# Optimization experiments

Hardware: AMD Instinct MI355X
Metric: run time of the kernel (lower is better)

## Reference

```python
import jax, jax.numpy as jnp
import numpy as np

B, DK, N, DV = 16, 64, 8192, 64


def setup_inputs() -> dict:
    key = jax.random.key(0)
    kq, kk, kv = jax.random.split(key, 3)
    q = jax.random.normal(kq, (B, DK, N), dtype=jnp.float32)   # channel-first q
    k = jax.random.normal(kk, (B, N, DK), dtype=jnp.float32)
    v = jax.random.normal(kv, (B, N, DV), dtype=jnp.float32)
    return {"q": q, "k": k, "v": v}


def reference(q, k, v):
    # torch: bmm(q.permute(0,2,1), bmm(k.permute(0,2,1), v))
    # k^T v: [B, DK, DV] -- small on-chip-able intermediate
    ktv = jnp.einsum('bnk,bnv->bkv', k, v)
    # q^T (k^T v): [B, N, DV]
    out = jnp.einsum('bkn,bkv->bnv', q, ktv)
    return out
```

## Files before the change

kernel.cpp:

```cpp
#include <hip/hip_runtime.h>


#define B_   16
#define N_   8192
#define DK_  64
#define DV_  64

__global__ __launch_bounds__(256) void p1_partial(
    const float* __restrict__ K, const float* __restrict__ V,
    float* __restrict__ part, int rows_per_chunk)
{
    const int c = blockIdx.x;
    const int b = blockIdx.y;
    const int t = threadIdx.x;
    const int n0 = c * rows_per_chunk;

    const float* Kb = K + ((size_t)b * N_ + n0) * DK_;
    const float* Vb = V + ((size_t)b * N_ + n0) * DV_;

    __shared__ float sK[64 * 64];
    __shared__ float sV[64 * 64];

    const int kk4 = (t >> 4) * 4;
    const int vv4 = (t & 15) * 4;

    float acc[4][4] = {};

    for (int s = 0; s < rows_per_chunk; s += 64) {
        const float4* Ks = (const float4*)(Kb + (size_t)s * DK_);
        const float4* Vs = (const float4*)(Vb + (size_t)s * DV_);
        float4* sK4 = (float4*)sK;
        float4* sV4 = (float4*)sV;
        __syncthreads();
        #pragma unroll
        for (int i = t; i < 1024; i += 256) {
            sK4[i] = Ks[i];
            sV4[i] = Vs[i];
        }
        __syncthreads();

        #pragma unroll 8
        for (int n = 0; n < 64; ++n) {
            const float4 fk = *(const float4*)&sK[n * 64 + kk4];
            const float4 fv = *(const float4*)&sV[n * 64 + vv4];
            acc[0][0] += fk.x * fv.x; acc[0][1] += fk.x * fv.y;
            acc[0][2] += fk.x * fv.z; acc[0][3] += fk.x * fv.w;
            acc[1][0] += fk.y * fv.x; acc[1][1] += fk.y * fv.y;
            acc[1][2] += fk.y * fv.z; acc[1][3] += fk.y * fv.w;
            acc[2][0] += fk.z * fv.x; acc[2][1] += fk.z * fv.y;
            acc[2][2] += fk.z * fv.z; acc[2][3] += fk.z * fv.w;
            acc[3][0] += fk.w * fv.x; acc[3][1] += fk.w * fv.y;
            acc[3][2] += fk.w * fv.z; acc[3][3] += fk.w * fv.w;
        }
    }

    float* P = part + ((size_t)c * B_ + b) * 4096;
    #pragma unroll
    for (int i = 0; i < 4; ++i) {
        *(float4*)&P[(kk4 + i) * 64 + vv4] =
            make_float4(acc[i][0], acc[i][1], acc[i][2], acc[i][3]);
    }
}

__global__ __launch_bounds__(256) void p1_reduce(
    const float* __restrict__ part, float* __restrict__ ktv, int chunks)
{
    const int i = blockIdx.x * 256 + threadIdx.x;
    float4 s = make_float4(0.f, 0.f, 0.f, 0.f);
    for (int c = 0; c < chunks; ++c) {
        const float4 p = ((const float4*)part)[(size_t)c * 16384 + i];
        s.x += p.x; s.y += p.y; s.z += p.z; s.w += p.w;
    }
    ((float4*)ktv)[i] = s;
}

__global__ __launch_bounds__(256) void p2(
    const float* __restrict__ q, const float* __restrict__ ktv,
    float* __restrict__ out)
{
    const int nb = blockIdx.x;
    const int b  = blockIdx.y;
    const int t  = threadIdx.x;
    const int n0 = nb * 128;

    __shared__ float qs[64 * 128];
    __shared__ float ks[64 * 64];

    const float4* kt4 = (const float4*)(ktv + (size_t)b * 4096);
    #pragma unroll
    for (int i = t; i < 1024; i += 256) ((float4*)ks)[i] = kt4[i];

    const float* qb = q + (size_t)b * DK_ * N_ + n0;
    #pragma unroll
    for (int i = t; i < 2048; i += 256) {
        const int k  = i >> 5;
        const int c4 = i & 31;
        ((float4*)&qs[k * 128])[c4] = *(const float4*)&qb[(size_t)k * N_ + c4 * 4];
    }
    __syncthreads();

    const int nl = (t >> 4) * 8;
    const int vl = (t & 15) * 4;

    float acc[8][4] = {};

    #pragma unroll 4
    for (int k = 0; k < 64; ++k) {
        const float4 kv = *(const float4*)&ks[k * 64 + vl];
        float qn[8];
        *(float4*)&qn[0] = *(const float4*)&qs[k * 128 + nl];
        *(float4*)&qn[4] = *(const float4*)&qs[k * 128 + nl + 4];
        #pragma unroll
        for (int i = 0; i < 8; ++i) {
            acc[i][0] += qn[i] * kv.x;
            acc[i][1] += qn[i] * kv.y;
            acc[i][2] += qn[i] * kv.z;
            acc[i][3] += qn[i] * kv.w;
        }
    }

    float* ob = out + ((size_t)b * N_ + n0 + nl) * DV_ + vl;
    #pragma unroll
    for (int i = 0; i < 8; ++i) {
        *(float4*)&ob[(size_t)i * DV_] =
            make_float4(acc[i][0], acc[i][1], acc[i][2], acc[i][3]);
    }
}

extern "C" void kernel_launch(void* const* d_in, const int* in_sizes, int n_in,
                              void* d_out, int out_size, void* d_ws, size_t ws_size,
                              hipStream_t stream)
{
    const float* q = (const float*)d_in[0];
    const float* k = (const float*)d_in[1];
    const float* v = (const float*)d_in[2];
    float* out = (float*)d_out;

    int chunks = 32;
    while (chunks > 1 &&
           (size_t)(chunks + 1) * B_ * 4096 * sizeof(float) > ws_size)
        chunks >>= 1;
    const int rows_per_chunk = N_ / chunks;

    float* part = (float*)d_ws;
    float* ktv  = part + (size_t)chunks * B_ * 4096;

    p1_partial<<<dim3(chunks, B_), 256, 0, stream>>>(k, v, part, rows_per_chunk);
    p1_reduce<<<dim3(64), 256, 0, stream>>>(part, ktv, chunks);
    p2<<<dim3(64, B_), 256, 0, stream>>>(q, ktv, out);
}
```

Baseline: 161.3 us.

## Use 8x8 register tiles, double-buffered K/V loads and in-block wave reduction

```diff
diff --git a/kernel.cpp b/kernel.cpp
--- a/kernel.cpp
+++ b/kernel.cpp
@@ -1,73 +1,108 @@
 #include <hip/hip_runtime.h>
 
 
-#define B_   16
-#define N_   8192
-#define DK_  64
-#define DV_  64
+#define B_      16
+#define N_      8192
+#define DK_     64
+#define DV_     64
+#define CHUNKS_ 32
+#define ROWS_   256
+#define SUB_    4
 
 __global__ __launch_bounds__(256) void p1_partial(
     const float* __restrict__ K, const float* __restrict__ V,
-    float* __restrict__ part, int rows_per_chunk)
+    float* __restrict__ part)
 {
-    const int c = blockIdx.x;
-    const int b = blockIdx.y;
-    const int t = threadIdx.x;
-    const int n0 = c * rows_per_chunk;
+    __shared__ float sm[4][4096];
 
-    const float* Kb = K + ((size_t)b * N_ + n0) * DK_;
-    const float* Vb = V + ((size_t)b * N_ + n0) * DV_;
+    const int c = blockIdx.x, b = blockIdx.y, t = threadIdx.x;
+    const int w = t >> 6, lane = t & 63;
+    const int kk = (lane >> 3) * 8;
+    const int vv = (lane & 7) * 8;
 
-    __shared__ float sK[64 * 64];
-    __shared__ float sV[64 * 64];
+    const float4* K4 = (const float4*)(K + ((size_t)b * N_ + (size_t)c * ROWS_) * DK_);
+    const float4* V4 = (const float4*)(V + ((size_t)b * N_ + (size_t)c * ROWS_) * DV_);
 
-    const int kk4 = (t >> 4) * 4;
-    const int vv4 = (t & 15) * 4;
+    #pragma unroll
+    for (int j = 0; j < 4; ++j) {
+        ((float4*)sm[0])[t + 256 * j] = K4[t + 256 * j];
+        ((float4*)sm[1])[t + 256 * j] = V4[t + 256 * j];
+    }
+    __syncthreads();
 
-    float acc[4][4] = {};
+    float acc[8][8] = {};
 
-    for (int s = 0; s < rows_per_chunk; s += 64) {
-        const float4* Ks = (const float4*)(Kb + (size_t)s * DK_);
-        const float4* Vs = (const float4*)(Vb + (size_t)s * DV_);
-        float4* sK4 = (float4*)sK;
-        float4* sV4 = (float4*)sV;
-        __syncthreads();
+    for (int s = 0; s < SUB_; ++s) {
+        float4 nk[4], nv[4];
+        if (s + 1 < SUB_) {
+            const float4* Kn = K4 + (size_t)(s + 1) * 1024;
+            const float4* Vn = V4 + (size_t)(s + 1) * 1024;
+            #pragma unroll
+            for (int j = 0; j < 4; ++j) {
+                nk[j] = Kn[t + 256 * j];
+                nv[j] = Vn[t + 256 * j];
+            }
+        }
+
+        const float* cK = sm[(s & 1) * 2];
+        const float* cV = sm[(s & 1) * 2 + 1];
         #pragma unroll
-        for (int i = t; i < 1024; i += 256) {
-            sK4[i] = Ks[i];
-            sV4[i] = Vs[i];
+        for (int rr = 0; rr < 16; ++rr) {
+            const int r = w * 16 + rr;
+            alignas(16) float fk[8], fv[8];
+            *(float4*)&fk[0] = *(const float4*)&cK[r * 64 + kk];
+            *(float4*)&fk[4] = *(const float4*)&cK[r * 64 + kk + 4];
+            *(float4*)&fv[0] = *(const float4*)&cV[r * 64 + vv];
+            *(float4*)&fv[4] = *(const float4*)&cV[r * 64 + vv + 4];
+            #pragma unroll
+            for (int i = 0; i < 8; ++i)
+                #pragma unroll
+                for (int j = 0; j < 8; ++j)
+                    acc[i][j] += fk[i] * fv[j];
+        }
+
+        if (s + 1 < SUB_) {
+            float* wK = sm[((s + 1) & 1) * 2];
+            float* wV = sm[((s + 1) & 1) * 2 + 1];
+            #pragma unroll
+            for (int j = 0; j < 4; ++j) {
+                ((float4*)wK)[t + 256 * j] = nk[j];
+                ((float4*)wV)[t + 256 * j] = nv[j];
+            }
         }
         __syncthreads();
-
-        #pragma unroll 8
-        for (int n = 0; n < 64; ++n) {
-            const float4 fk = *(const float4*)&sK[n * 64 + kk4];
-            const float4 fv = *(const float4*)&sV[n * 64 + vv4];
-            acc[0][0] += fk.x * fv.x; acc[0][1] += fk.x * fv.y;
-            acc[0][2] += fk.x * fv.z; acc[0][3] += fk.x * fv.w;
-            acc[1][0] += fk.y * fv.x; acc[1][1] += fk.y * fv.y;
-            acc[1][2] += fk.y * fv.z; acc[1][3] += fk.y * fv.w;
-            acc[2][0] += fk.z * fv.x; acc[2][1] += fk.z * fv.y;
-            acc[2][2] += fk.z * fv.z; acc[2][3] += fk.z * fv.w;
-            acc[3][0] += fk.w * fv.x; acc[3][1] += fk.w * fv.y;
-            acc[3][2] += fk.w * fv.z; acc[3][3] += fk.w * fv.w;
-        }
     }
 
-    float* P = part + ((size_t)c * B_ + b) * 4096;
+    float* reg = sm[w];
     #pragma unroll
-    for (int i = 0; i < 4; ++i) {
-        *(float4*)&P[(kk4 + i) * 64 + vv4] =
-            make_float4(acc[i][0], acc[i][1], acc[i][2], acc[i][3]);
+    for (int i = 0; i < 8; ++i) {
+        *(float4*)&reg[(kk + i) * 64 + vv]     = make_float4(acc[i][0], acc[i][1], acc[i][2], acc[i][3]);
+        *(float4*)&reg[(kk + i) * 64 + vv + 4] = make_float4(acc[i][4], acc[i][5], acc[i][6], acc[i][7]);
+    }
+    __syncthreads();
+
+    float4* P = (float4*)(part + ((size_t)c * B_ + b) * 4096);
+    #pragma unroll
+    for (int j = 0; j < 4; ++j) {
+        const int idx = t + 256 * j;
+        const float4 s0 = ((const float4*)sm[0])[idx];
+        const float4 s1 = ((const float4*)sm[1])[idx];
+        const float4 s2 = ((const float4*)sm[2])[idx];
+        const float4 s3 = ((const float4*)sm[3])[idx];
+        P[idx] = make_float4(s0.x + s1.x + s2.x + s3.x,
+                             s0.y + s1.y + s2.y + s3.y,
+                             s0.z + s1.z + s2.z + s3.z,
+                             s0.w + s1.w + s2.w + s3.w);
     }
 }
 
 __global__ __launch_bounds__(256) void p1_reduce(
-    const float* __restrict__ part, float* __restrict__ ktv, int chunks)
+    const float* __restrict__ part, float* __restrict__ ktv)
 {
     const int i = blockIdx.x * 256 + threadIdx.x;
     float4 s = make_float4(0.f, 0.f, 0.f, 0.f);
-    for (int c = 0; c < chunks; ++c) {
+    #pragma unroll
+    for (int c = 0; c < CHUNKS_; ++c) {
         const float4 p = ((const float4*)part)[(size_t)c * 16384 + i];
         s.x += p.x; s.y += p.y; s.z += p.z; s.w += p.w;
     }
@@ -78,52 +113,49 @@
     const float* __restrict__ q, const float* __restrict__ ktv,
     float* __restrict__ out)
 {
-    const int nb = blockIdx.x;
-    const int b  = blockIdx.y;
-    const int t  = threadIdx.x;
-    const int n0 = nb * 128;
+    __shared__ float qs[64 * 256];
+    __shared__ float ks[64 * 64];
 
-    __shared__ float qs[64 * 128];
-    __shared__ float ks[64 * 64];
+    const int nb = blockIdx.x, b = blockIdx.y, t = threadIdx.x;
+    const int n0 = nb * 256;
+    const int nl = (t >> 3) * 8;
+    const int vl = (t & 7) * 8;
 
     const float4* kt4 = (const float4*)(ktv + (size_t)b * 4096);
     #pragma unroll
-    for (int i = t; i < 1024; i += 256) ((float4*)ks)[i] = kt4[i];
+    for (int j = 0; j < 4; ++j)
+        ((float4*)ks)[t + 256 * j] = kt4[t + 256 * j];
 
     const float* qb = q + (size_t)b * DK_ * N_ + n0;
     #pragma unroll
-    for (int i = t; i < 2048; i += 256) {
-        const int k  = i >> 5;
-        const int c4 = i & 31;
-        ((float4*)&qs[k * 128])[c4] = *(const float4*)&qb[(size_t)k * N_ + c4 * 4];
+    for (int j = 0; j < 16; ++j) {
+        const int i  = t + 256 * j;
+        const int k  = i >> 6;
+        const int c4 = i & 63;
+        ((float4*)&qs[k * 256])[c4] = ((const float4*)&qb[(size_t)k * N_])[c4];
     }
     __syncthreads();
 
-    const int nl = (t >> 4) * 8;
-    const int vl = (t & 15) * 4;
-
-    float acc[8][4] = {};
-
+    float acc[8][8] = {};
     #pragma unroll 4
     for (int k = 0; k < 64; ++k) {
-        const float4 kv = *(const float4*)&ks[k * 64 + vl];
-        float qn[8];
-        *(float4*)&qn[0] = *(const float4*)&qs[k * 128 + nl];
-        *(float4*)&qn[4] = *(const float4*)&qs[k * 128 + nl + 4];
+        alignas(16) float qn[8], kv[8];
+        *(float4*)&qn[0] = *(const float4*)&qs[k * 256 + nl];
+        *(float4*)&qn[4] = *(const float4*)&qs[k * 256 + nl + 4];
+        *(float4*)&kv[0] = *(const float4*)&ks[k * 64 + vl];
+        *(float4*)&kv[4] = *(const float4*)&ks[k * 64 + vl + 4];
         #pragma unroll
-        for (int i = 0; i < 8; ++i) {
-            acc[i][0] += qn[i] * kv.x;
-            acc[i][1] += qn[i] * kv.y;
-            acc[i][2] += qn[i] * kv.z;
-            acc[i][3] += qn[i] * kv.w;
-        }
+        for (int i = 0; i < 8; ++i)
+            #pragma unroll
+            for (int j = 0; j < 8; ++j)
+                acc[i][j] += qn[i] * kv[j];
     }
 
     float* ob = out + ((size_t)b * N_ + n0 + nl) * DV_ + vl;
     #pragma unroll
     for (int i = 0; i < 8; ++i) {
-        *(float4*)&ob[(size_t)i * DV_] =
-            make_float4(acc[i][0], acc[i][1], acc[i][2], acc[i][3]);
+        *(float4*)&ob[(size_t)i * DV_]     = make_float4(acc[i][0], acc[i][1], acc[i][2], acc[i][3]);
+        *(float4*)&ob[(size_t)i * DV_ + 4] = make_float4(acc[i][4], acc[i][5], acc[i][6], acc[i][7]);
     }
 }
 
@@ -131,21 +163,16 @@
                               void* d_out, int out_size, void* d_ws, size_t ws_size,
                               hipStream_t stream)
 {
+    (void)in_sizes; (void)n_in; (void)out_size; (void)ws_size;
     const float* q = (const float*)d_in[0];
     const float* k = (const float*)d_in[1];
     const float* v = (const float*)d_in[2];
     float* out = (float*)d_out;
 
-    int chunks = 32;
-    while (chunks > 1 &&
-           (size_t)(chunks + 1) * B_ * 4096 * sizeof(float) > ws_size)
-        chunks >>= 1;
-    const int rows_per_chunk = N_ / chunks;
+    float* part = (float*)d_ws;
+    float* ktv  = part + (size_t)CHUNKS_ * B_ * 4096;
 
-    float* part = (float*)d_ws;
-    float* ktv  = part + (size_t)chunks * B_ * 4096;
-
-    p1_partial<<<dim3(chunks, B_), 256, 0, stream>>>(k, v, part, rows_per_chunk);
-    p1_reduce<<<dim3(64), 256, 0, stream>>>(part, ktv, chunks);
-    p2<<<dim3(64, B_), 256, 0, stream>>>(q, ktv, out);
+    p1_partial<<<dim3(CHUNKS_, B_), 256, 0, stream>>>(k, v, part);
+    p1_reduce<<<dim3(64), 256, 0, stream>>>(part, ktv);
+    p2<<<dim3(32, B_), 256, 0, stream>>>(q, ktv, out);
 }
```

New measurement: 175.0 us. 1.08x slower.
